# Kernel optimization log

Hardware: AMD Instinct MI355X
Metric: run time of the kernel (lower is better)

Reference implementation:

```python
import jax, jax.numpy as jnp
import numpy as np

N_NODES = 50000
N_EDGES = 800000
ATOM_DIM = 32
EDGE_DIM = 16
HIDDEN = 64
NUM_STEPS = 3
NUM_GRAPHS = 256
OUT_DIM = 1


def setup_inputs() -> dict:
    key = jax.random.key(0)
    ks = jax.random.split(key, 20)
    s = 0.05
    inp = {
        "x": jax.random.normal(ks[0], (N_NODES, ATOM_DIM), dtype=jnp.float32),
        "edge_index": jax.random.randint(ks[1], (2, N_EDGES), 0, N_NODES),
        "edge_attr": jax.random.normal(ks[2], (N_EDGES, EDGE_DIM), dtype=jnp.float32),
        "batch": jnp.sort(jax.random.randint(ks[3], (N_NODES,), 0, NUM_GRAPHS)),
        # atom embedding
        "W_embed": jax.random.normal(ks[4], (ATOM_DIM, HIDDEN)) * s,
        "b_embed": jnp.zeros((HIDDEN,)),
        # message MLP: Linear(2H+E, H) -> ReLU -> Linear(H, H)
        "W_m1": jax.random.normal(ks[5], (2 * HIDDEN + EDGE_DIM, HIDDEN)) * s,
        "b_m1": jnp.zeros((HIDDEN,)),
        "W_m2": jax.random.normal(ks[6], (HIDDEN, HIDDEN)) * s,
        "b_m2": jnp.zeros((HIDDEN,)),
        # GRUCell (torch layout: [3H, in] stacked r,z,n)
        "W_ih": jax.random.normal(ks[7], (3 * HIDDEN, HIDDEN)) * s,
        "b_ih": jnp.zeros((3 * HIDDEN,)),
        "W_hh": jax.random.normal(ks[8], (3 * HIDDEN, HIDDEN)) * s,
        "b_hh": jnp.zeros((3 * HIDDEN,)),
        # head: Linear(2H, H) -> ReLU -> Linear(H, out)
        "W_h1": jax.random.normal(ks[9], (2 * HIDDEN, HIDDEN)) * s,
        "b_h1": jnp.zeros((HIDDEN,)),
        "W_h2": jax.random.normal(ks[10], (HIDDEN, OUT_DIM)) * s,
        "b_h2": jnp.zeros((OUT_DIM,)),
    }
    return inp


def _gru_cell(inp, h, W_ih, b_ih, W_hh, b_hh):
    gi = inp @ W_ih.T + b_ih   # [N, 3H]
    gh = h @ W_hh.T + b_hh     # [N, 3H]
    i_r, i_z, i_n = jnp.split(gi, 3, axis=-1)
    h_r, h_z, h_n = jnp.split(gh, 3, axis=-1)
    r = jax.nn.sigmoid(i_r + h_r)
    z = jax.nn.sigmoid(i_z + h_z)
    n = jnp.tanh(i_n + r * h_n)
    return (1.0 - z) * n + z * h


def reference(x, edge_index, edge_attr, batch,
              W_embed, b_embed, W_m1, b_m1, W_m2, b_m2,
              W_ih, b_ih, W_hh, b_hh, W_h1, b_h1, W_h2, b_h2):
    h = x @ W_embed + b_embed                       # [N, H]
    src, dst = edge_index[0], edge_index[1]         # PyG: x_j = x[src], x_i = x[dst]
    for _ in range(NUM_STEPS):                      # tied weights
        m = jnp.concatenate([h[src], h[dst], edge_attr], axis=-1)  # [E, 2H+ED]
        m = jax.nn.relu(m @ W_m1 + b_m1) @ W_m2 + b_m2             # [E, H]
        agg = jax.ops.segment_sum(m, dst, num_segments=N_NODES)    # scatter-add
        h = _gru_cell(agg, h, W_ih, b_ih, W_hh, b_hh)
    g_sum = jax.ops.segment_sum(h, batch, num_segments=NUM_GRAPHS)  # [G, H]
    cnt = jax.ops.segment_sum(jnp.ones((N_NODES,), h.dtype), batch,
                              num_segments=NUM_GRAPHS)
    g_mean = g_sum / jnp.maximum(cnt, 1.0)[:, None]
    g = jnp.concatenate([g_sum, g_mean], axis=-1)   # [G, 2H]
    return jax.nn.relu(g @ W_h1 + b_h1) @ W_h2 + b_h2  # [G, out]
```

## Files before the change

### kernel.cpp

```cpp
#include <hip/hip_runtime.h>
#include <math.h>

#define NN 50000
#define NE 800000
#define AD 32
#define ED 16
#define HD 64
#define NG 256
#define NTILES (NE / 16)
#define EGRID 1280
#define TPX (NTILES / 8)
#define GGRID 768
#define GTILES (NN / 16)
#define PGRID 782
#define SGRID 1024
#define HGRID 1024
#define EPGRID 1024
#define NPX (NN / 8)

typedef short bf16x8 __attribute__((ext_vector_type(8)));
typedef float f32x4  __attribute__((ext_vector_type(4)));
union U4B { uint4 u; bf16x8 v; };

__device__ __forceinline__ float blo(unsigned u){ return __uint_as_float(u << 16); }
__device__ __forceinline__ float bhi(unsigned u){ return __uint_as_float(u & 0xffff0000u); }
__device__ __forceinline__ unsigned short f2bf(float f){
  unsigned u = __float_as_uint(f);
  u += 0x7fffu + ((u >> 16) & 1u);
  return (unsigned short)(u >> 16);
}
__device__ __forceinline__ unsigned packbf2(float a, float b){
  return (unsigned)f2bf(a) | ((unsigned)f2bf(b) << 16);
}
__device__ __forceinline__ bf16x8 ldfrag_g(const unsigned* p){
  U4B x; x.u = *(const uint4*)p; return x.v;
}
__device__ __forceinline__ unsigned srp1(unsigned a, unsigned b, unsigned c){
  float lo = fmaxf(blo(a) + blo(b) + blo(c), 0.f);
  float hi = fmaxf(bhi(a) + bhi(b) + bhi(c), 0.f);
  return packbf2(lo, hi);
}
__device__ __forceinline__ bf16x8 srp4(uint4 a, uint4 b, uint4 c){
  U4B r;
  r.u.x = srp1(a.x, b.x, c.x);
  r.u.y = srp1(a.y, b.y, c.y);
  r.u.z = srp1(a.z, b.z, c.z);
  r.u.w = srp1(a.w, b.w, c.w);
  return r.v;
}

__global__ __launch_bounds__(256) void k_prep(const float* __restrict__ W1,
                                              const float* __restrict__ W2,
                                              const float* __restrict__ Wih,
                                              const float* __restrict__ Whh,
                                              const float* __restrict__ b1,
                                              unsigned short* __restrict__ W1Tp,
                                              unsigned short* __restrict__ W2Tp,
                                              unsigned short* __restrict__ Wgru,
                                              unsigned short* __restrict__ W1cTp)
{
  int idx = blockIdx.x * 256 + threadIdx.x;
  if (idx < 64 * 168){
    int n = idx / 168, k = idx % 168;
    W1Tp[idx] = (k < 144) ? f2bf(W1[k * 64 + n]) : (unsigned short)0;
    return;
  }
  idx -= 64 * 168;
  if (idx < 64 * 72){
    int n = idx / 72, k = idx % 72;
    W2Tp[idx] = (k < 64) ? f2bf(W2[k * 64 + n]) : (unsigned short)0;
    return;
  }
  idx -= 64 * 72;
  if (idx < 384 * 64){
    int j = idx & 7;
    int g = (idx >> 3) % 384;
    int blk = idx >> 3; blk /= 384;
    int q = blk & 3, ks = blk >> 2;
    int k = ks * 32 + q * 8 + j;
    float v = (g < 192) ? Wih[g * 64 + k] : Whh[(g - 192) * 64 + k];
    Wgru[idx] = f2bf(v);
    return;
  }
  idx -= 384 * 64;
  if (idx < 64 * 32){
    int n = idx / 32, k = idx % 32;
    float v = (k < 16) ? W1[(128 + k) * 64 + n] : (k == 16 ? b1[n] : 0.f);
    W1cTp[idx] = f2bf(v);
  }
}

__global__ __launch_bounds__(256) void k_hist(const int* __restrict__ eidx, int* __restrict__ deg)
{
  const int g = blockIdx.x & 7, bi = blockIdx.x >> 3;
  const int lo = g * NPX, hi = lo + NPX;
  for (int e = bi * 256 + threadIdx.x; e < NE; e += (HGRID / 8) * 256){
    int d = eidx[NE + e];
    if (d >= lo && d < hi) atomicAdd(&deg[d], 1);
  }
}

__global__ __launch_bounds__(1024) void k_scan1(const int* __restrict__ deg,
                                                int* __restrict__ cur,
                                                int* __restrict__ bsum)
{
  __shared__ int s[1024];
  const int t = threadIdx.x;
  const int idx = blockIdx.x * 1024 + t;
  int v = (idx < NN) ? deg[idx] : 0;
  s[t] = v;
  __syncthreads();
  for (int d = 1; d < 1024; d <<= 1){
    int y = (t >= d) ? s[t - d] : 0;
    __syncthreads();
    s[t] += y;
    __syncthreads();
  }
  if (idx < NN) cur[idx] = s[t] - v;
  if (t == 1023) bsum[blockIdx.x] = s[1023];
}

__global__ __launch_bounds__(64) void k_scan2(const int* __restrict__ bsum,
                                              int* __restrict__ bpre)
{
  const int t = threadIdx.x;
  const int nb = (NN + 1023) / 1024;
  int v = (t < nb) ? bsum[t] : 0;
  int orig = v;
  #pragma unroll
  for (int off = 1; off < 64; off <<= 1){
    int u = __shfl_up(v, off);
    if (t >= off) v += u;
  }
  if (t < nb) bpre[t] = v - orig;
}

__global__ __launch_bounds__(1024) void k_scan3(int* __restrict__ cur,
                                                const int* __restrict__ bpre)
{
  const int idx = blockIdx.x * 1024 + threadIdx.x;
  if (idx < NN) cur[idx] += bpre[blockIdx.x];
}

__global__ __launch_bounds__(256) void k_scatter(const int* __restrict__ eidx,
                                                 int* __restrict__ cur,
                                                 int4* __restrict__ sde)
{
  const int g = blockIdx.x & 7, bi = blockIdx.x >> 3;
  const int lo = g * NPX, hi = lo + NPX;
  for (int e = bi * 256 + threadIdx.x; e < NE; e += (SGRID / 8) * 256){
    int d = eidx[NE + e];
    if (d >= lo && d < hi){
      int s = eidx[e];
      int p = atomicAdd(&cur[d], 1);
      sde[p] = make_int4(s, d, e, 0);
    }
  }
}

__global__ __launch_bounds__(256) void k_eprep(const int4* __restrict__ sde,
                                               const float* __restrict__ eattr,
                                               const unsigned* __restrict__ W1cTp32,
                                               unsigned* __restrict__ E1s,
                                               int2* __restrict__ sd8)
{
  const int t = threadIdx.x, lane = t & 63, wv = t >> 6;
  const int m = lane & 15, q = lane >> 4;
  bf16x8 wf[4];
  #pragma unroll
  for (int tl = 0; tl < 4; ++tl)
    wf[tl] = ldfrag_g(W1cTp32 + (tl * 16 + m) * 16 + q * 4);

  for (int wt = blockIdx.x * 4 + wv; wt < NTILES; wt += EPGRID * 4){
    const int base = wt * 16;
    int4 rec = sde[base + m];
    if (q == 0) sd8[base + m] = make_int2(rec.x, rec.y);
    U4B x;
    if (q < 2){
      const float* ea = eattr + (size_t)rec.z * 16 + q * 8;
      float4 v0 = *(const float4*)(ea);
      float4 v1 = *(const float4*)(ea + 4);
      x.u.x = packbf2(v0.x, v0.y); x.u.y = packbf2(v0.z, v0.w);
      x.u.z = packbf2(v1.x, v1.y); x.u.w = packbf2(v1.z, v1.w);
    } else if (q == 2) x.u = make_uint4(0x3F80u, 0, 0, 0);
    else               x.u = make_uint4(0, 0, 0, 0);
    bf16x8 a = x.v;
    f32x4 c[4];
    #pragma unroll
    for (int tl = 0; tl < 4; ++tl) c[tl] = f32x4{0.f,0.f,0.f,0.f};
    #pragma unroll
    for (int tl = 0; tl < 4; ++tl)
      c[tl] = __builtin_amdgcn_mfma_f32_16x16x32_bf16(a, wf[tl], c[tl], 0, 0, 0);
    #pragma unroll
    for (int tl = 0; tl < 4; ++tl){
      #pragma unroll
      for (int rr = 0; rr < 4; ++rr){
        float v = c[tl][rr];
        float pp = __shfl_xor(v, 1);
        if (!(m & 1))
          E1s[(size_t)(base + q * 4 + rr) * 32 + (tl * 16 + m) / 2] = packbf2(v, pp);
      }
    }
  }
}

__global__ __launch_bounds__(256, 4) void k_pre(const unsigned* __restrict__ h_bf,
                                                const unsigned short* __restrict__ W1Tp,
                                                unsigned* __restrict__ C12)
{
  const int t = threadIdx.x, lane = t & 63, wv = t >> 6;
  const int m = lane & 15, q = lane >> 4;
  bf16x8 wa[4][2], wb[4][2];
  #pragma unroll
  for (int tl = 0; tl < 4; ++tl)
    #pragma unroll
    for (int ks = 0; ks < 2; ++ks){
      wa[tl][ks] = ldfrag_g((const unsigned*)(W1Tp + (tl * 16 + m) * 168 + ks * 32 + q * 8));
      wb[tl][ks] = ldfrag_g((const unsigned*)(W1Tp + (tl * 16 + m) * 168 + 64 + ks * 32 + q * 8));
    }
  for (int wt = blockIdx.x * 4 + wv; wt < GTILES; wt += PGRID * 4){
    const int n0 = wt * 16;
    bf16x8 aH[2];
    #pragma unroll
    for (int ks = 0; ks < 2; ++ks)
      aH[ks] = ldfrag_g(h_bf + (size_t)(n0 + m) * 32 + ks * 16 + q * 4);
    f32x4 ca[4], cb[4];
    #pragma unroll
    for (int tl = 0; tl < 4; ++tl){ ca[tl] = f32x4{0.f,0.f,0.f,0.f}; cb[tl] = ca[tl]; }
    #pragma unroll
    for (int ks = 0; ks < 2; ++ks)
      #pragma unroll
      for (int tl = 0; tl < 4; ++tl){
        ca[tl] = __builtin_amdgcn_mfma_f32_16x16x32_bf16(aH[ks], wa[tl][ks], ca[tl], 0, 0, 0);
        cb[tl] = __builtin_amdgcn_mfma_f32_16x16x32_bf16(aH[ks], wb[tl][ks], cb[tl], 0, 0, 0);
      }
    #pragma unroll
    for (int tl = 0; tl < 4; ++tl){
      #pragma unroll
      for (int rr = 0; rr < 4; ++rr){
        const int node = n0 + q * 4 + rr;
        float va = ca[tl][rr], vb = cb[tl][rr];
        float pa = __shfl_xor(va, 1), pb = __shfl_xor(vb, 1);
        if (!(m & 1)){
          C12[(size_t)node * 64 + (tl * 16 + m) / 2]      = packbf2(va, pa);
          C12[(size_t)node * 64 + 32 + (tl * 16 + m) / 2] = packbf2(vb, pb);
        }
      }
    }
  }
}

__global__ __launch_bounds__(256) void k_embed(const float* __restrict__ x,
                                               const float* __restrict__ We,
                                               const float* __restrict__ be,
                                               float* __restrict__ h,
                                               unsigned* __restrict__ h_bf,
                                               float* __restrict__ agg)
{
  const int t = threadIdx.x;
  const int j = t & 63, nd = t >> 6;
  const int node = blockIdx.x * 4 + nd;
  const float* xr = x + (size_t)node * AD;
  float acc = be[j];
  #pragma unroll 8
  for (int k = 0; k < AD; ++k)
    acc += xr[k] * We[k * HD + j];
  h[(size_t)node * HD + j] = acc;
  agg[(size_t)node * HD + j] = 0.f;
  float p = __shfl_down(acc, 1);
  if (!(j & 1)) h_bf[(size_t)node * 32 + (j >> 1)] = packbf2(acc, p);
}

__global__ __launch_bounds__(256, 4) void k_edge(const unsigned* __restrict__ C12,
                                                 const unsigned* __restrict__ E1s,
                                                 const int2* __restrict__ sd8,
                                                 const unsigned* __restrict__ W2Tp32,
                                                 const float* __restrict__ b2,
                                                 float* __restrict__ agg)
{
  const int t = threadIdx.x;
  const int lane = t & 63, wv = t >> 6;
  const int m = lane & 15, q = lane >> 4;

  bf16x8 w2f[4][2];
  #pragma unroll
  for (int tl = 0; tl < 4; ++tl)
    #pragma unroll
    for (int ks = 0; ks < 2; ++ks)
      w2f[tl][ks] = ldfrag_g(W2Tp32 + (tl * 16 + m) * 36 + ks * 16 + q * 4);

  float b2v[4];
  #pragma unroll
  for (int tl = 0; tl < 4; ++tl) b2v[tl] = b2[tl * 16 + m];

  const int xcd = blockIdx.x & 7, bi = blockIdx.x >> 3;
  const int wend = (xcd + 1) * TPX;
  const int wstep = (EGRID / 8) * 4;
  int wt = xcd * TPX + bi * 4 + wv;

  int2 cursd = sd8[wt * 16 + m];

  while (wt < wend){
    const int wn = wt + wstep;
    const bool hasn = (wn < wend);
    int2 nsd = make_int2(0, 0);
    if (hasn) nsd = sd8[wn * 16 + m];

    const int scur = cursd.x, dcur = cursd.y;

    const unsigned* c1p = C12 + (size_t)scur * 64;
    const unsigned* c2p = C12 + (size_t)dcur * 64 + 32;
    const unsigned* e1p = E1s + (size_t)(wt * 16 + m) * 32;
    uint4 c1a = *(const uint4*)(c1p + q * 4);
    uint4 c1b = *(const uint4*)(c1p + 16 + q * 4);
    uint4 c2a = *(const uint4*)(c2p + q * 4);
    uint4 c2b = *(const uint4*)(c2p + 16 + q * 4);
    uint4 e1a = *(const uint4*)(e1p + q * 4);
    uint4 e1b = *(const uint4*)(e1p + 16 + q * 4);

    bf16x8 af0 = srp4(c1a, c2a, e1a);
    bf16x8 af1 = srp4(c1b, c2b, e1b);

    f32x4 o0 = {0.f,0.f,0.f,0.f}, o1 = o0, o2 = o0, o3 = o0;
    o0 = __builtin_amdgcn_mfma_f32_16x16x32_bf16(af0, w2f[0][0], o0, 0, 0, 0);
    o1 = __builtin_amdgcn_mfma_f32_16x16x32_bf16(af0, w2f[1][0], o1, 0, 0, 0);
    o2 = __builtin_amdgcn_mfma_f32_16x16x32_bf16(af0, w2f[2][0], o2, 0, 0, 0);
    o3 = __builtin_amdgcn_mfma_f32_16x16x32_bf16(af0, w2f[3][0], o3, 0, 0, 0);
    o0 = __builtin_amdgcn_mfma_f32_16x16x32_bf16(af1, w2f[0][1], o0, 0, 0, 0);
    o1 = __builtin_amdgcn_mfma_f32_16x16x32_bf16(af1, w2f[1][1], o1, 0, 0, 0);
    o2 = __builtin_amdgcn_mfma_f32_16x16x32_bf16(af1, w2f[2][1], o2, 0, 0, 0);
    o3 = __builtin_amdgcn_mfma_f32_16x16x32_bf16(af1, w2f[3][1], o3, 0, 0, 0);

    int prev = __shfl_up(dcur, 1);
    bool isStart = (m == 0) || (dcur != prev);
    unsigned long long bal = __ballot(isStart);
    unsigned bs = (unsigned)bal & 0xFFFFu;
    int nr = __popc(bs);
    unsigned rem = bs & (bs - 1);
    int lo = 0;
    for (int r = 0; r < nr; ++r){
      int hi = rem ? (__ffs(rem) - 1) : 16;
      rem &= rem - 1;
      float s0 = 0.f, s1 = 0.f, s2 = 0.f, s3 = 0.f;
      #pragma unroll
      for (int rr = 0; rr < 4; ++rr){
        int row = q * 4 + rr;
        bool in = (row >= lo) && (row < hi);
        s0 += in ? o0[rr] : 0.f;
        s1 += in ? o1[rr] : 0.f;
        s2 += in ? o2[rr] : 0.f;
        s3 += in ? o3[rr] : 0.f;
      }
      s0 += __shfl_xor(s0, 16); s0 += __shfl_xor(s0, 32);
      s1 += __shfl_xor(s1, 16); s1 += __shfl_xor(s1, 32);
      s2 += __shfl_xor(s2, 16); s2 += __shfl_xor(s2, 32);
      s3 += __shfl_xor(s3, 16); s3 += __shfl_xor(s3, 32);
      int d = __shfl(dcur, lo);
      float cntf = (float)(hi - lo);
      if (q == 0){
        float v0 = s0 + cntf * b2v[0];
        float v1 = s1 + cntf * b2v[1];
        float v2 = s2 + cntf * b2v[2];
        float v3 = s3 + cntf * b2v[3];
        float* dp = &agg[(size_t)d * HD + m];
        if (r == 0 || r == nr - 1){
          atomicAdd(dp +  0, v0); atomicAdd(dp + 16, v1);
          atomicAdd(dp + 32, v2); atomicAdd(dp + 48, v3);
        } else {
          dp[ 0] = v0; dp[16] = v1; dp[32] = v2; dp[48] = v3;
        }
      }
      lo = hi;
    }

    wt = wn; cursd = nsd;
  }
}

__global__ __launch_bounds__(256) void k_gru(float* __restrict__ agg,
                                             float* __restrict__ h,
                                             unsigned* __restrict__ h_bf,
                                             const unsigned short* __restrict__ Wgru,
                                             const float* __restrict__ bih,
                                             const float* __restrict__ bhh)
{
  __shared__ __align__(16) unsigned short sWg[384 * 64];

  const int t = threadIdx.x;
  {
    const uint4* srcp = (const uint4*)Wgru;
    uint4* dstp = (uint4*)sWg;
    for (int i = t; i < 384 * 64 * 2 / 16; i += 256) dstp[i] = srcp[i];
  }
  __syncthreads();

  const int lane = t & 63, wv = t >> 6;
  const int m = lane & 15, q = lane >> 4;

  float bi_r[4], bi_z[4], bi_n[4], bh_r[4], bh_z[4], bh_n[4];
  #pragma unroll
  for (int tl = 0; tl < 4; ++tl){
    bi_r[tl] = bih[tl * 16 + m];  bi_z[tl] = bih[64 + tl * 16 + m];  bi_n[tl] = bih[128 + tl * 16 + m];
    bh_r[tl] = bhh[tl * 16 + m];  bh_z[tl] = bhh[64 + tl * 16 + m];  bh_n[tl] = bhh[128 + tl * 16 + m];
  }

  for (int wt = blockIdx.x * 4 + wv; wt < GTILES; wt += GGRID * 4){
    const int n0 = wt * 16;

    bf16x8 aA[2], aH[2];
    #pragma unroll
    for (int ks = 0; ks < 2; ++ks){
      const float* ap = agg + (size_t)(n0 + m) * 64 + ks * 32 + q * 8;
      float4 v0 = *(const float4*)ap;
      float4 v1 = *(const float4*)(ap + 4);
      U4B x;
      x.u.x = packbf2(v0.x, v0.y); x.u.y = packbf2(v0.z, v0.w);
      x.u.z = packbf2(v1.x, v1.y); x.u.w = packbf2(v1.z, v1.w);
      aA[ks] = x.v;
      aH[ks] = ldfrag_g(h_bf + (size_t)(n0 + m) * 32 + ks * 16 + q * 4);
    }

    f32x4 ci[12], ch[12];
    #pragma unroll
    for (int tl = 0; tl < 12; ++tl){ ci[tl] = f32x4{0.f,0.f,0.f,0.f}; ch[tl] = ci[tl]; }
    #pragma unroll
    for (int ks = 0; ks < 2; ++ks){
      #pragma unroll
      for (int tl = 0; tl < 12; ++tl){
        bf16x8 bi = *(const bf16x8*)&sWg[((ks * 4 + q) * 384 + tl * 16 + m) * 8];
        ci[tl] = __builtin_amdgcn_mfma_f32_16x16x32_bf16(aA[ks], bi, ci[tl], 0, 0, 0);
        bf16x8 bh = *(const bf16x8*)&sWg[((ks * 4 + q) * 384 + 192 + tl * 16 + m) * 8];
        ch[tl] = __builtin_amdgcn_mfma_f32_16x16x32_bf16(aH[ks], bh, ch[tl], 0, 0, 0);
      }
    }

    #pragma unroll
    for (int tl = 0; tl < 4; ++tl){
      #pragma unroll
      for (int rr = 0; rr < 4; ++rr){
        const int node = n0 + q * 4 + rr;
        float ir = ci[tl][rr]     + bi_r[tl], hr = ch[tl][rr]     + bh_r[tl];
        float iz = ci[4 + tl][rr] + bi_z[tl], hz = ch[4 + tl][rr] + bh_z[tl];
        float in_ = ci[8 + tl][rr] + bi_n[tl], hn = ch[8 + tl][rr] + bh_n[tl];
        float rg = 1.f / (1.f + __expf(-(ir + hr)));
        float zg = 1.f / (1.f + __expf(-(iz + hz)));
        float ng = tanhf(in_ + rg * hn);
        float hold = h[(size_t)node * HD + tl * 16 + m];
        float hnew = (1.f - zg) * ng + zg * hold;
        h[(size_t)node * HD + tl * 16 + m] = hnew;
        agg[(size_t)node * HD + tl * 16 + m] = 0.f;
        float pp = __shfl_xor(hnew, 1);
        if (!(m & 1))
          h_bf[(size_t)node * 32 + tl * 8 + (m >> 1)] = packbf2(hnew, pp);
      }
    }
  }
}

__global__ __launch_bounds__(256) void k_pool(const float* __restrict__ h,
                                              const int* __restrict__ batch,
                                              float* __restrict__ gsum,
                                              float* __restrict__ cnt)
{
  const int t = threadIdx.x;
  const int j = t & 63, r = t >> 6;
  const int n0 = blockIdx.x * 64 + r * 16;
  float acc = 0.f, c = 0.f;
  int cur = -1;
  for (int i = 0; i < 16; ++i){
    int n = n0 + i;
    if (n >= NN) break;
    int g = batch[n];
    if (g != cur){
      if (cur >= 0){
        atomicAdd(&gsum[cur * HD + j], acc);
        if (j == 0) atomicAdd(&cnt[cur], c);
      }
      cur = g; acc = 0.f; c = 0.f;
    }
    acc += h[(size_t)n * HD + j];
    c += 1.f;
  }
  if (cur >= 0){
    atomicAdd(&gsum[cur * HD + j], acc);
    if (j == 0) atomicAdd(&cnt[cur], c);
  }
}

__global__ __launch_bounds__(64) void k_head(const float* __restrict__ gsum,
                                             const float* __restrict__ cnt,
                                             const float* __restrict__ W1,
                                             const float* __restrict__ b1,
                                             const float* __restrict__ W2,
                                             const float* __restrict__ b2,
                                             float* __restrict__ out)
{
  __shared__ float gv[128];
  const int g = blockIdx.x, j = threadIdx.x;
  float s = gsum[g * HD + j];
  float c = cnt[g];
  gv[j] = s;
  gv[64 + j] = s / fmaxf(c, 1.f);
  __syncthreads();
  float acc = b1[j];
  #pragma unroll 8
  for (int k = 0; k < 128; ++k)
    acc += gv[k] * W1[k * HD + j];
  acc = fmaxf(acc, 0.f);
  float v = acc * W2[j];
  #pragma unroll
  for (int off = 32; off; off >>= 1) v += __shfl_down(v, off, 64);
  if (j == 0) out[g] = v + b2[0];
}

extern "C" void kernel_launch(void* const* d_in, const int* in_sizes, int n_in,
                              void* d_out, int out_size, void* d_ws, size_t ws_size,
                              hipStream_t stream)
{
  (void)in_sizes; (void)n_in; (void)out_size; (void)ws_size;
  const float* x     = (const float*)d_in[0];
  const int*   eidx  = (const int*)d_in[1];
  const float* eattr = (const float*)d_in[2];
  const int*   batch = (const int*)d_in[3];
  const float* We    = (const float*)d_in[4];
  const float* be    = (const float*)d_in[5];
  const float* Wm1   = (const float*)d_in[6];
  const float* bm1   = (const float*)d_in[7];
  const float* Wm2   = (const float*)d_in[8];
  const float* bm2   = (const float*)d_in[9];
  const float* Wih   = (const float*)d_in[10];
  const float* bih   = (const float*)d_in[11];
  const float* Whh   = (const float*)d_in[12];
  const float* bhh   = (const float*)d_in[13];
  const float* Wh1   = (const float*)d_in[14];
  const float* bh1   = (const float*)d_in[15];
  const float* Wh2   = (const float*)d_in[16];
  const float* bh2   = (const float*)d_in[17];

  char* w = (char*)d_ws;
  float* h     = (float*)w;                      w += (size_t)NN * HD * 4;
  unsigned* h_bf = (unsigned*)w;                 w += (size_t)NN * 32 * 4;
  float* agg   = (float*)w;                      w += (size_t)NN * HD * 4;
  int*   deg   = (int*)w;                        w += (size_t)NN * 4;
  int*   cur   = (int*)w;                        w += (size_t)NN * 4;
  int4*  sde   = (int4*)w;                       w += (size_t)NE * 16;
  int2*  sd8   = (int2*)w;                       w += (size_t)NE * 8;
  int*   bsum  = (int*)w;                        w += 64 * 4;
  int*   bpre  = (int*)w;                        w += 64 * 4;
  unsigned short* W1Tp = (unsigned short*)w;     w += 64 * 168 * 2;
  unsigned short* W2Tp = (unsigned short*)w;     w += 64 * 72 * 2;
  unsigned short* Wgru = (unsigned short*)w;     w += 384 * 64 * 2;
  unsigned short* W1cTp = (unsigned short*)w;    w += 64 * 32 * 2 + 192;
  float* gsum  = (float*)w;                      w += (size_t)NG * HD * 4;
  float* cnt   = (float*)w;                      w += (size_t)NG * 4;
  unsigned* C12 = (unsigned*)w;                  w += (size_t)NN * 64 * 4;
  unsigned* E1s = (unsigned*)w;                  w += (size_t)NE * 32 * 4;

  const int nscanb = (NN + 1023) / 1024;

  k_prep<<<164, 256, 0, stream>>>(Wm1, Wm2, Wih, Whh, bm1, W1Tp, W2Tp, Wgru, W1cTp);
  hipMemsetAsync(deg, 0, (size_t)NN * 4, stream);
  k_hist<<<HGRID, 256, 0, stream>>>(eidx, deg);
  k_scan1<<<nscanb, 1024, 0, stream>>>(deg, cur, bsum);
  k_scan2<<<1, 64, 0, stream>>>(bsum, bpre);
  k_scan3<<<nscanb, 1024, 0, stream>>>(cur, bpre);
  k_scatter<<<SGRID, 256, 0, stream>>>(eidx, cur, sde);
  k_eprep<<<EPGRID, 256, 0, stream>>>(sde, eattr, (const unsigned*)W1cTp, E1s, sd8);

  k_embed<<<NN / 4, 256, 0, stream>>>(x, We, be, h, h_bf, agg);
  for (int s = 0; s < 3; ++s){
    k_pre<<<PGRID, 256, 0, stream>>>(h_bf, W1Tp, C12);
    k_edge<<<EGRID, 256, 0, stream>>>(C12, E1s, sd8, (const unsigned*)W2Tp, bm2, agg);
    k_gru<<<GGRID, 256, 0, stream>>>(agg, h, h_bf, Wgru, bih, bhh);
  }
  hipMemsetAsync(gsum, 0, (size_t)(NG * HD + NG) * 4, stream);
  k_pool<<<(NN + 63) / 64, 256, 0, stream>>>(h, batch, gsum, cnt);
  k_head<<<NG, 64, 0, stream>>>(gsum, cnt, Wh1, bh1, Wh2, bh2, (float*)d_out);
}
```

Measured before the change: 600.3 us.

## Recompute edge-attr projection inside edge kernel instead of storing E1s

The precomputed per-edge first-layer projection (64 bf16 per edge) is no longer stored in a large buffer. A sorted bf16 copy of the raw edge attributes (16 values per edge) is stored instead, and the edge kernel recomputes the projection with an extra MFMA per tile, passing it through per-wave LDS. This cuts per-step edge-side global reads by about 4x, at the cost of extra MFMA work, LDS traffic and LDS allocation in the hot edge kernel across all three steps.

After: 568.1 us. 5.4% less time.

```diff
diff --git a/kernel.cpp b/kernel.cpp
--- a/kernel.cpp
+++ b/kernel.cpp
@@ -15,7 +15,6 @@
 #define PGRID 782
 #define SGRID 1024
 #define HGRID 1024
-#define EPGRID 1024
 #define NPX (NN / 8)
 
 typedef short bf16x8 __attribute__((ext_vector_type(8)));
@@ -158,50 +157,27 @@
   }
 }
 
-__global__ __launch_bounds__(256) void k_eprep(const int4* __restrict__ sde,
+__global__ __launch_bounds__(256) void k_esort(const int4* __restrict__ sde,
                                                const float* __restrict__ eattr,
-                                               const unsigned* __restrict__ W1cTp32,
-                                               unsigned* __restrict__ E1s,
-                                               int2* __restrict__ sd8)
-{
-  const int t = threadIdx.x, lane = t & 63, wv = t >> 6;
-  const int m = lane & 15, q = lane >> 4;
-  bf16x8 wf[4];
-  #pragma unroll
-  for (int tl = 0; tl < 4; ++tl)
-    wf[tl] = ldfrag_g(W1cTp32 + (tl * 16 + m) * 16 + q * 4);
-
-  for (int wt = blockIdx.x * 4 + wv; wt < NTILES; wt += EPGRID * 4){
-    const int base = wt * 16;
-    int4 rec = sde[base + m];
-    if (q == 0) sd8[base + m] = make_int2(rec.x, rec.y);
-    U4B x;
-    if (q < 2){
-      const float* ea = eattr + (size_t)rec.z * 16 + q * 8;
-      float4 v0 = *(const float4*)(ea);
-      float4 v1 = *(const float4*)(ea + 4);
-      x.u.x = packbf2(v0.x, v0.y); x.u.y = packbf2(v0.z, v0.w);
-      x.u.z = packbf2(v1.x, v1.y); x.u.w = packbf2(v1.z, v1.w);
-    } else if (q == 2) x.u = make_uint4(0x3F80u, 0, 0, 0);
-    else               x.u = make_uint4(0, 0, 0, 0);
-    bf16x8 a = x.v;
-    f32x4 c[4];
-    #pragma unroll
-    for (int tl = 0; tl < 4; ++tl) c[tl] = f32x4{0.f,0.f,0.f,0.f};
-    #pragma unroll
-    for (int tl = 0; tl < 4; ++tl)
-      c[tl] = __builtin_amdgcn_mfma_f32_16x16x32_bf16(a, wf[tl], c[tl], 0, 0, 0);
-    #pragma unroll
-    for (int tl = 0; tl < 4; ++tl){
-      #pragma unroll
-      for (int rr = 0; rr < 4; ++rr){
-        float v = c[tl][rr];
-        float pp = __shfl_xor(v, 1);
-        if (!(m & 1))
-          E1s[(size_t)(base + q * 4 + rr) * 32 + (tl * 16 + m) / 2] = packbf2(v, pp);
-      }
-    }
-  }
+                                               int2* __restrict__ sd8,
+                                               unsigned* __restrict__ eattr_s)
+{
+  int p = blockIdx.x * 256 + threadIdx.x;
+  if (p >= NE) return;
+  int4 rec = sde[p];
+  sd8[p] = make_int2(rec.x, rec.y);
+  const float* ea = eattr + (size_t)rec.z * 16;
+  float4 v0 = *(const float4*)(ea);
+  float4 v1 = *(const float4*)(ea + 4);
+  float4 v2 = *(const float4*)(ea + 8);
+  float4 v3 = *(const float4*)(ea + 12);
+  uint4 o0, o1;
+  o0.x = packbf2(v0.x, v0.y); o0.y = packbf2(v0.z, v0.w);
+  o0.z = packbf2(v1.x, v1.y); o0.w = packbf2(v1.z, v1.w);
+  o1.x = packbf2(v2.x, v2.y); o1.y = packbf2(v2.z, v2.w);
+  o1.z = packbf2(v3.x, v3.y); o1.w = packbf2(v3.z, v3.w);
+  *(uint4*)(eattr_s + (size_t)p * 8)     = o0;
+  *(uint4*)(eattr_s + (size_t)p * 8 + 4) = o1;
 }
 
 __global__ __launch_bounds__(256, 4) void k_pre(const unsigned* __restrict__ h_bf,
@@ -272,12 +248,15 @@
 }
 
 __global__ __launch_bounds__(256, 4) void k_edge(const unsigned* __restrict__ C12,
-                                                 const unsigned* __restrict__ E1s,
+                                                 const unsigned* __restrict__ eattr_s,
                                                  const int2* __restrict__ sd8,
                                                  const unsigned* __restrict__ W2Tp32,
+                                                 const unsigned* __restrict__ W1cTp32,
                                                  const float* __restrict__ b2,
                                                  float* __restrict__ agg)
 {
+  __shared__ __align__(16) unsigned short sE1[4][16 * 72];
+
   const int t = threadIdx.x;
   const int lane = t & 63, wv = t >> 6;
   const int m = lane & 15, q = lane >> 4;
@@ -289,9 +268,16 @@
     for (int ks = 0; ks < 2; ++ks)
       w2f[tl][ks] = ldfrag_g(W2Tp32 + (tl * 16 + m) * 36 + ks * 16 + q * 4);
 
+  bf16x8 wf[4];
+  #pragma unroll
+  for (int tl = 0; tl < 4; ++tl)
+    wf[tl] = ldfrag_g(W1cTp32 + (tl * 16 + m) * 16 + q * 4);
+
   float b2v[4];
   #pragma unroll
   for (int tl = 0; tl < 4; ++tl) b2v[tl] = b2[tl * 16 + m];
+
+  unsigned short* sE1w = sE1[wv];
 
   const int xcd = blockIdx.x & 7, bi = blockIdx.x >> 3;
   const int wend = (xcd + 1) * TPX;
@@ -308,15 +294,34 @@
 
     const int scur = cursd.x, dcur = cursd.y;
 
+    U4B ea;
+    if (q < 2)      ea.u = *(const uint4*)(eattr_s + (size_t)(wt * 16 + m) * 8 + q * 4);
+    else if (q == 2) ea.u = make_uint4(0x3F80u, 0, 0, 0);
+    else             ea.u = make_uint4(0, 0, 0, 0);
+    f32x4 e1t[4];
+    #pragma unroll
+    for (int tl = 0; tl < 4; ++tl){
+      e1t[tl] = f32x4{0.f,0.f,0.f,0.f};
+      e1t[tl] = __builtin_amdgcn_mfma_f32_16x16x32_bf16(wf[tl], ea.v, e1t[tl], 0, 0, 0);
+    }
+    {
+      unsigned* row = (unsigned*)(sE1w + m * 72);
+      #pragma unroll
+      for (int tl = 0; tl < 4; ++tl){
+        row[tl * 8 + q * 2 + 0] = packbf2(e1t[tl][0], e1t[tl][1]);
+        row[tl * 8 + q * 2 + 1] = packbf2(e1t[tl][2], e1t[tl][3]);
+      }
+    }
+
     const unsigned* c1p = C12 + (size_t)scur * 64;
     const unsigned* c2p = C12 + (size_t)dcur * 64 + 32;
-    const unsigned* e1p = E1s + (size_t)(wt * 16 + m) * 32;
     uint4 c1a = *(const uint4*)(c1p + q * 4);
     uint4 c1b = *(const uint4*)(c1p + 16 + q * 4);
     uint4 c2a = *(const uint4*)(c2p + q * 4);
     uint4 c2b = *(const uint4*)(c2p + 16 + q * 4);
-    uint4 e1a = *(const uint4*)(e1p + q * 4);
-    uint4 e1b = *(const uint4*)(e1p + 16 + q * 4);
+
+    uint4 e1a = *(const uint4*)(sE1w + m * 72 + q * 8);
+    uint4 e1b = *(const uint4*)(sE1w + m * 72 + 32 + q * 8);
 
     bf16x8 af0 = srp4(c1a, c2a, e1a);
     bf16x8 af1 = srp4(c1b, c2b, e1b);
@@ -545,6 +550,7 @@
   int*   cur   = (int*)w;                        w += (size_t)NN * 4;
   int4*  sde   = (int4*)w;                       w += (size_t)NE * 16;
   int2*  sd8   = (int2*)w;                       w += (size_t)NE * 8;
+  unsigned* eattr_s = (unsigned*)w;              w += (size_t)NE * 8 * 4;
   int*   bsum  = (int*)w;                        w += 64 * 4;
   int*   bpre  = (int*)w;                        w += 64 * 4;
   unsigned short* W1Tp = (unsigned short*)w;     w += 64 * 168 * 2;
@@ -554,7 +560,6 @@
   float* gsum  = (float*)w;                      w += (size_t)NG * HD * 4;
   float* cnt   = (float*)w;                      w += (size_t)NG * 4;
   unsigned* C12 = (unsigned*)w;                  w += (size_t)NN * 64 * 4;
-  unsigned* E1s = (unsigned*)w;                  w += (size_t)NE * 32 * 4;
 
   const int nscanb = (NN + 1023) / 1024;
 
@@ -565,12 +570,13 @@
   k_scan2<<<1, 64, 0, stream>>>(bsum, bpre);
   k_scan3<<<nscanb, 1024, 0, stream>>>(cur, bpre);
   k_scatter<<<SGRID, 256, 0, stream>>>(eidx, cur, sde);
-  k_eprep<<<EPGRID, 256, 0, stream>>>(sde, eattr, (const unsigned*)W1cTp, E1s, sd8);
+  k_esort<<<(NE + 255) / 256, 256, 0, stream>>>(sde, eattr, sd8, eattr_s);
 
   k_embed<<<NN / 4, 256, 0, stream>>>(x, We, be, h, h_bf, agg);
   for (int s = 0; s < 3; ++s){
     k_pre<<<PGRID, 256, 0, stream>>>(h_bf, W1Tp, C12);
-    k_edge<<<EGRID, 256, 0, stream>>>(C12, E1s, sd8, (const unsigned*)W2Tp, bm2, agg);
+    k_edge<<<EGRID, 256, 0, stream>>>(C12, eattr_s, sd8, (const unsigned*)W2Tp,
+                                      (const unsigned*)W1cTp, bm2, agg);
     k_gru<<<GGRID, 256, 0, stream>>>(agg, h, h_bf, Wgru, bih, bhh);
   }
   hipMemsetAsync(gsum, 0, (size_t)(NG * HD + NG) * 4, stream);
```
